# Kernel optimization log

Measured on AMD Instinct MI355X. Metric: run time of the kernel, lower is better.

## Reference

```python
import jax, jax.numpy as jnp
import numpy as np

MAX_H = 64
MAX_W = 64

def setup_inputs() -> dict:
    key = jax.random.key(0)
    ks = jax.random.split(key, 6)
    in_f, out_f = 128, 128
    x0 = jax.random.normal(ks[0], (32, 64, 64, in_f), dtype=jnp.float32)
    x1 = jax.random.normal(ks[1], (32, 32, 64, in_f), dtype=jnp.float32)
    x2 = jax.random.normal(ks[2], (32, 64, 32, in_f), dtype=jnp.float32)
    x3 = jax.random.normal(ks[3], (32, 32, 32, in_f), dtype=jnp.float32)
    stdv = 1.0 / np.sqrt(in_f)
    weight = jax.random.uniform(ks[4], (out_f, in_f), minval=-stdv, maxval=stdv, dtype=jnp.float32)
    bias = jax.random.uniform(ks[5], (out_f,), minval=-stdv, maxval=stdv, dtype=jnp.float32)
    return {"x0": x0, "x1": x1, "x2": x2, "x3": x3, "weight": weight, "bias": bias}

def reference(x0, x1, x2, x3, weight, bias):
    # Grouped/ragged linear: flatten each variable-shaped tensor to rows of
    # in_features, concatenate, apply shared y = x @ W^T + b, then reshape to
    # (-1, max_H, max_W, out_features) as in the original CUDA path.
    k = weight.shape[0]
    flat = jnp.concatenate([x.reshape(-1, x.shape[-1]) for x in (x0, x1, x2, x3)], axis=0)
    out = flat @ weight.T + bias  # [total_rows, out_features]
    return out.reshape(-1, MAX_H, MAX_W, k)
```

## Files before the change

kernel.cpp:

```cpp
#include <hip/hip_runtime.h>
#include <hip/hip_bf16.h>


typedef __attribute__((ext_vector_type(8))) short bf8_t;
typedef __attribute__((ext_vector_type(4))) float f4_t;

typedef const unsigned __attribute__((address_space(1)))* gp_t;
typedef unsigned __attribute__((address_space(3)))* lp_t;

__device__ __forceinline__ short bfc(float f) {
    return __builtin_bit_cast(short, __float2bfloat16(f));
}

#define SEG0 131072L
#define SEG1 196608L
#define SEG2 262144L

__device__ __forceinline__ const float* tile_src(long gr,
    const float* __restrict__ x0, const float* __restrict__ x1,
    const float* __restrict__ x2, const float* __restrict__ x3)
{
    const float* xp; long loc;
    if      (gr < SEG0) { xp = x0; loc = gr; }
    else if (gr < SEG1) { xp = x1; loc = gr - SEG0; }
    else if (gr < SEG2) { xp = x2; loc = gr - SEG1; }
    else                { xp = x3; loc = gr - SEG2; }
    return xp + loc * 128;
}

__device__ __forceinline__ void stage_tile(const float* __restrict__ src,
                                           float* __restrict__ buf,
                                           int wave, int lane)
{
#pragma unroll
    for (int i = 0; i < 8; ++i) {
        const int c  = i * 256 + wave * 64 + lane;
        const int r  = c >> 5;
        const int kc = c & 31;
        const float* g = src + r * 128 + ((kc ^ (r & 7)) << 2);
        float* l = buf + (i * 256 + wave * 64) * 4;
        __builtin_amdgcn_global_load_lds((gp_t)g, (lp_t)l, 16, 0, 0);
    }
}

__device__ __forceinline__ void compute_tile(const float* __restrict__ buf,
    float* __restrict__ obase, const bf8_t (&wf)[2][4],
    f4_t bf0, f4_t bf1, int wave, int lm, int lk)
{
#pragma unroll
    for (int s = 0; s < 4; ++s) {
        const int row = s * 16 + lm;
        const int sw  = row & 7;
        f4_t raw[8];
#pragma unroll
        for (int ks = 0; ks < 4; ++ks) {
            const int c0 = ks * 8 + lk * 2;
            raw[2*ks]   = *reinterpret_cast<const f4_t*>(buf + row * 128 + (((c0    ) ^ sw) << 2));
            raw[2*ks+1] = *reinterpret_cast<const f4_t*>(buf + row * 128 + (((c0 + 1) ^ sw) << 2));
        }
        bf8_t xf[4];
#pragma unroll
        for (int ks = 0; ks < 4; ++ks) {
            f4_t a = raw[2*ks], b = raw[2*ks+1];
            bf8_t t;
            t[0]=bfc(a.x); t[1]=bfc(a.y); t[2]=bfc(a.z); t[3]=bfc(a.w);
            t[4]=bfc(b.x); t[5]=bfc(b.y); t[6]=bfc(b.z); t[7]=bfc(b.w);
            xf[ks] = t;
        }
        f4_t acc0 = bf0, acc1 = bf1;
#pragma unroll
        for (int ks = 0; ks < 4; ++ks) {
            acc0 = __builtin_amdgcn_mfma_f32_16x16x32_bf16(wf[0][ks], xf[ks], acc0, 0, 0, 0);
            acc1 = __builtin_amdgcn_mfma_f32_16x16x32_bf16(wf[1][ks], xf[ks], acc1, 0, 0, 0);
        }
        float* orow = obase + (long)row * 128 + wave * 32 + lk * 4;
        __builtin_nontemporal_store(acc0, reinterpret_cast<f4_t*>(orow));
        __builtin_nontemporal_store(acc1, reinterpret_cast<f4_t*>(orow + 16));
    }
}

__global__ __launch_bounds__(256)
void lin_kernel(const float* __restrict__ x0, const float* __restrict__ x1,
                const float* __restrict__ x2, const float* __restrict__ x3,
                const float* __restrict__ W, const float* __restrict__ bias,
                float* __restrict__ out)
{
    __shared__ float xb0[64 * 128];
    __shared__ float xb1[64 * 128];

    const int tid  = threadIdx.x;
    const int wave = tid >> 6;
    const int lane = tid & 63;
    const int lm   = lane & 15;
    const int lk   = lane >> 4;

    const long blk0 = (long)blockIdx.x * 576;

    stage_tile(tile_src(blk0, x0, x1, x2, x3), xb0, wave, lane);

    bf8_t wf[2][4];
#pragma unroll
    for (int nt = 0; nt < 2; ++nt) {
        const int nW = wave * 32 + nt * 16 + lm;
#pragma unroll
        for (int ks = 0; ks < 4; ++ks) {
            const float* p = W + nW * 128 + ks * 32 + lk * 8;
            f4_t a = *reinterpret_cast<const f4_t*>(p);
            f4_t b = *reinterpret_cast<const f4_t*>(p + 4);
            bf8_t t;
            t[0]=bfc(a.x); t[1]=bfc(a.y); t[2]=bfc(a.z); t[3]=bfc(a.w);
            t[4]=bfc(b.x); t[5]=bfc(b.y); t[6]=bfc(b.z); t[7]=bfc(b.w);
            wf[nt][ks] = t;
        }
    }
    const f4_t bf0 = *reinterpret_cast<const f4_t*>(bias + wave * 32 +      lk * 4);
    const f4_t bf1 = *reinterpret_cast<const f4_t*>(bias + wave * 32 + 16 + lk * 4);

    asm volatile("s_waitcnt vmcnt(0)" ::: "memory");
    __builtin_amdgcn_s_barrier();

    float* cur = xb0;
    float* nxt = xb1;
#pragma unroll 1
    for (int t = 0; t < 9; ++t) {
        if (t < 8)
            stage_tile(tile_src(blk0 + (t + 1) * 64, x0, x1, x2, x3), nxt, wave, lane);
        compute_tile(cur, out + (blk0 + t * 64) * 128, wf, bf0, bf1, wave, lm, lk);
        if (t < 8) {
            asm volatile("s_waitcnt vmcnt(0)" ::: "memory");
            __builtin_amdgcn_s_barrier();
        }
        float* tmp = cur; cur = nxt; nxt = tmp;
    }
}

extern "C" void kernel_launch(void* const* d_in, const int* in_sizes, int n_in,
                              void* d_out, int out_size, void* d_ws, size_t ws_size,
                              hipStream_t stream) {
    const float* x0 = (const float*)d_in[0];
    const float* x1 = (const float*)d_in[1];
    const float* x2 = (const float*)d_in[2];
    const float* x3 = (const float*)d_in[3];
    const float* W  = (const float*)d_in[4];
    const float* b  = (const float*)d_in[5];
    float* out = (float*)d_out;

    hipLaunchKernelGGL(lin_kernel, dim3(512), dim3(256), 0, stream,
                       x0, x1, x2, x3, W, b, out);
}
```

Before: 65.81 us.

## Switch to triple-buffered 32-row tiles with deeper prefetch and more blocks

Shrinks the staged tile from 64 to 32 rows and keeps three LDS buffers, so two tiles are in flight while one is computed. Partial vmcnt waits replace the full drain. The grid grows from 512 to 768 blocks to improve occupancy and balance. Output stores change from nontemporal to regular stores, which may affect cache behaviour on the large output write. The vmcnt counts assume exact instruction counts, and the output stores also count toward vmcnt, which could make the waits inexact.

```diff
diff --git a/kernel.cpp b/kernel.cpp
--- a/kernel.cpp
+++ b/kernel.cpp
@@ -29,16 +29,15 @@
 }
 
 __device__ __forceinline__ void stage_tile(const float* __restrict__ src,
-                                           float* __restrict__ buf,
-                                           int wave, int lane)
+                                           float* __restrict__ buf, int tid)
 {
 #pragma unroll
-    for (int i = 0; i < 8; ++i) {
-        const int c  = i * 256 + wave * 64 + lane;
+    for (int i = 0; i < 4; ++i) {
+        const int c  = i * 256 + tid;
         const int r  = c >> 5;
         const int kc = c & 31;
         const float* g = src + r * 128 + ((kc ^ (r & 7)) << 2);
-        float* l = buf + (i * 256 + wave * 64) * 4;
+        float* l = buf + (c & ~63) * 4;
         __builtin_amdgcn_global_load_lds((gp_t)g, (lp_t)l, 16, 0, 0);
     }
 }
@@ -48,20 +47,15 @@
     f4_t bf0, f4_t bf1, int wave, int lm, int lk)
 {
 #pragma unroll
-    for (int s = 0; s < 4; ++s) {
+    for (int s = 0; s < 2; ++s) {
         const int row = s * 16 + lm;
         const int sw  = row & 7;
-        f4_t raw[8];
+        bf8_t xf[4];
 #pragma unroll
         for (int ks = 0; ks < 4; ++ks) {
             const int c0 = ks * 8 + lk * 2;
-            raw[2*ks]   = *reinterpret_cast<const f4_t*>(buf + row * 128 + (((c0    ) ^ sw) << 2));
-            raw[2*ks+1] = *reinterpret_cast<const f4_t*>(buf + row * 128 + (((c0 + 1) ^ sw) << 2));
-        }
-        bf8_t xf[4];
-#pragma unroll
-        for (int ks = 0; ks < 4; ++ks) {
-            f4_t a = raw[2*ks], b = raw[2*ks+1];
+            f4_t a = *reinterpret_cast<const f4_t*>(buf + row * 128 + (((c0    ) ^ sw) << 2));
+            f4_t b = *reinterpret_cast<const f4_t*>(buf + row * 128 + (((c0 + 1) ^ sw) << 2));
             bf8_t t;
             t[0]=bfc(a.x); t[1]=bfc(a.y); t[2]=bfc(a.z); t[3]=bfc(a.w);
             t[4]=bfc(b.x); t[5]=bfc(b.y); t[6]=bfc(b.z); t[7]=bfc(b.w);
@@ -74,8 +68,8 @@
             acc1 = __builtin_amdgcn_mfma_f32_16x16x32_bf16(wf[1][ks], xf[ks], acc1, 0, 0, 0);
         }
         float* orow = obase + (long)row * 128 + wave * 32 + lk * 4;
-        __builtin_nontemporal_store(acc0, reinterpret_cast<f4_t*>(orow));
-        __builtin_nontemporal_store(acc1, reinterpret_cast<f4_t*>(orow + 16));
+        *reinterpret_cast<f4_t*>(orow)      = acc0;
+        *reinterpret_cast<f4_t*>(orow + 16) = acc1;
     }
 }
 
@@ -85,8 +79,9 @@
                 const float* __restrict__ W, const float* __restrict__ bias,
                 float* __restrict__ out)
 {
-    __shared__ float xb0[64 * 128];
-    __shared__ float xb1[64 * 128];
+    __shared__ float sb0[32 * 128];
+    __shared__ float sb1[32 * 128];
+    __shared__ float sb2[32 * 128];
 
     const int tid  = threadIdx.x;
     const int wave = tid >> 6;
@@ -94,9 +89,7 @@
     const int lm   = lane & 15;
     const int lk   = lane >> 4;
 
-    const long blk0 = (long)blockIdx.x * 576;
-
-    stage_tile(tile_src(blk0, x0, x1, x2, x3), xb0, wave, lane);
+    const long blk0 = (long)blockIdx.x * 384;
 
     bf8_t wf[2][4];
 #pragma unroll
@@ -116,21 +109,25 @@
     const f4_t bf0 = *reinterpret_cast<const f4_t*>(bias + wave * 32 +      lk * 4);
     const f4_t bf1 = *reinterpret_cast<const f4_t*>(bias + wave * 32 + 16 + lk * 4);
 
-    asm volatile("s_waitcnt vmcnt(0)" ::: "memory");
+    float *pA = sb0, *pB = sb1, *pC = sb2;
+    stage_tile(tile_src(blk0 +  0, x0, x1, x2, x3), pA, tid);
+    stage_tile(tile_src(blk0 + 32, x0, x1, x2, x3), pB, tid);
+
+    asm volatile("s_waitcnt vmcnt(4)" ::: "memory");
     __builtin_amdgcn_s_barrier();
+    asm volatile("" ::: "memory");
+    stage_tile(tile_src(blk0 + 64, x0, x1, x2, x3), pC, tid);
+    compute_tile(pA, out + blk0 * 128, wf, bf0, bf1, wave, lm, lk);
 
-    float* cur = xb0;
-    float* nxt = xb1;
 #pragma unroll 1
-    for (int t = 0; t < 9; ++t) {
-        if (t < 8)
-            stage_tile(tile_src(blk0 + (t + 1) * 64, x0, x1, x2, x3), nxt, wave, lane);
-        compute_tile(cur, out + (blk0 + t * 64) * 128, wf, bf0, bf1, wave, lm, lk);
-        if (t < 8) {
-            asm volatile("s_waitcnt vmcnt(0)" ::: "memory");
-            __builtin_amdgcn_s_barrier();
-        }
-        float* tmp = cur; cur = nxt; nxt = tmp;
+    for (int t = 1; t < 12; ++t) {
+        asm volatile("s_waitcnt vmcnt(8)" ::: "memory");
+        __builtin_amdgcn_s_barrier();
+        asm volatile("" ::: "memory");
+        float* tmp = pA; pA = pB; pB = pC; pC = tmp;
+        if (t + 2 < 12)
+            stage_tile(tile_src(blk0 + (long)(t + 2) * 32, x0, x1, x2, x3), pC, tid);
+        compute_tile(pA, out + (blk0 + (long)t * 32) * 128, wf, bf0, bf1, wave, lm, lk);
     }
 }
 
@@ -145,6 +142,6 @@
     const float* b  = (const float*)d_in[5];
     float* out = (float*)d_out;
 
-    hipLaunchKernelGGL(lin_kernel, dim3(512), dim3(256), 0, stream,
+    hipLaunchKernelGGL(lin_kernel, dim3(768), dim3(256), 0, stream,
                        x0, x1, x2, x3, W, b, out);
 }
```

Measured after the change: 63.36 us. 1.04x faster.
